# Kernel optimization log

Measured on AMD Instinct MI355X. Metric: run time of the kernel, lower is better.

## Reference

```python
import jax, jax.numpy as jnp
import numpy as np
import math

N_HEAD = 16
N_KV_HEAD = 4
WINDOW = 512
EPS = 1e-6


def _rotate_half(t):
    t1, t2 = jnp.split(t, 2, axis=-1)
    return jnp.concatenate([-t2, t1], axis=-1)


def _rope_tables(T, head_dim):
    theta = 1.0 / (10000.0 ** (jnp.arange(0, head_dim, 2, dtype=jnp.float32) / head_dim))
    pos = jnp.arange(T, dtype=jnp.float32)
    freqs = jnp.outer(pos, theta)                      # [T, d/2]
    cos = jnp.concatenate([jnp.cos(freqs), jnp.cos(freqs)], axis=-1)  # [T, d]
    sin = jnp.concatenate([jnp.sin(freqs), jnp.sin(freqs)], axis=-1)
    return cos, sin


def setup_inputs() -> dict:
    key = jax.random.key(0)
    k1, k2, k3, k4 = jax.random.split(key, 4)
    B, T, C = 1, 2048, 1024
    kv_out = 2 * N_KV_HEAD * (C // N_HEAD)  # 512
    x = jax.random.normal(k1, (B, T, C), dtype=jnp.float32)
    Wq = jax.random.normal(k2, (C, C), dtype=jnp.float32) * 0.02
    Wkv = jax.random.normal(k3, (kv_out, C), dtype=jnp.float32) * 0.02
    Wproj = jax.random.normal(k4, (C, C), dtype=jnp.float32) * 0.02
    return {"x": x, "Wq": Wq, "Wkv": Wkv, "Wproj": Wproj}


def reference(x, Wq, Wkv, Wproj):
    B, T, C = x.shape
    H, KV = N_HEAD, N_KV_HEAD
    d = C // H
    n_rep = H // KV

    q = (x @ Wq.T).reshape(B, T, H, d).transpose(0, 2, 1, 3)     # [B,H,T,d]
    kv = x @ Wkv.T                                               # [B,T,2*KV*d]
    k, v = jnp.split(kv, 2, axis=2)
    k = k.reshape(B, T, KV, d).transpose(0, 2, 1, 3)             # [B,KV,T,d]
    v = v.reshape(B, T, KV, d).transpose(0, 2, 1, 3)

    # QK L2 normalization
    q = q / (jnp.linalg.norm(q, axis=-1, keepdims=True) + EPS)
    k = k / (jnp.linalg.norm(k, axis=-1, keepdims=True) + EPS)

    # RoPE
    cos, sin = _rope_tables(T, d)
    cos = cos[None, None]  # [1,1,T,d]
    sin = sin[None, None]
    q = q * cos + _rotate_half(q) * sin
    k = k * cos + _rotate_half(k) * sin

    # GQA: repeat KV heads (repeat_interleave on head dim)
    k = jnp.repeat(k, n_rep, axis=1)   # [B,H,T,d]
    v = jnp.repeat(v, n_rep, axis=1)

    # sliding-window causal mask: cols <= rows and cols > rows - WINDOW
    rows = jnp.arange(T)[:, None]
    cols = jnp.arange(T)[None, :]
    mask = (cols <= rows) & (cols > rows - WINDOW)  # [T,T] bool

    scale = 1.0 / math.sqrt(d)
    scores = jnp.einsum("bhqd,bhkd->bhqk", q, k) * scale
    scores = jnp.where(mask[None, None], scores, -jnp.inf)
    attn = jax.nn.softmax(scores, axis=-1)
    y = jnp.einsum("bhqk,bhkd->bhqd", attn, v)      # [B,H,T,d]
    y = y.transpose(0, 2, 1, 3).reshape(B, T, C)
    return y @ Wproj.T
```

## Files before the change

kernel.cpp:

```cpp
#include <hip/hip_runtime.h>

#define T_SEQ 2048
#define C_DIM 1024
#define NH    16
#define NKV   4
#define HD    64
#define WIN   512

typedef __bf16 bf16x8 __attribute__((ext_vector_type(8)));
typedef __bf16 bf16x4 __attribute__((ext_vector_type(4)));
typedef float f32x4 __attribute__((ext_vector_type(4)));

#define MFMA16(a, b, c) __builtin_amdgcn_mfma_f32_16x16x32_bf16(a, b, c, 0, 0, 0)

#define GLD16(g, s)                                                          \
  __builtin_amdgcn_global_load_lds(                                          \
      (const __attribute__((address_space(1))) void*)(g),                    \
      (__attribute__((address_space(3))) void*)(s), 16, 0, 0)

__global__ __launch_bounds__(256) void prep_kernel(const float* __restrict__ x,
                                                   const float* __restrict__ Wq,
                                                   const float* __restrict__ Wkv,
                                                   const float* __restrict__ Wp,
                                                   __bf16* __restrict__ xb,
                                                   __bf16* __restrict__ Wqkvb,
                                                   __bf16* __restrict__ Wpb,
                                                   float2* __restrict__ ropeT) {
  int b = blockIdx.x;
  if (b >= 4608) {
    int idx = (b - 4608) * 256 + threadIdx.x;
    int t = idx >> 5, i = idx & 31;
    float theta = exp2f(-(float)i * (13.287712379549449f / 32.0f));
    float s, c;
    sincosf((float)t * theta, &s, &c);
    ropeT[idx] = make_float2(c, s);
    return;
  }
  const float* src;
  __bf16* dst;
  int off;
  if (b < 2048)      { src = x;   dst = xb;                off = b; }
  else if (b < 3072) { src = Wq;  dst = Wqkvb;             off = b - 2048; }
  else if (b < 3584) { src = Wkv; dst = Wqkvb + (1 << 20); off = b - 3072; }
  else               { src = Wp;  dst = Wpb;               off = b - 3584; }
  int i = off * 1024 + threadIdx.x * 4;
  float4 v = *(const float4*)(src + i);
  bf16x4 o;
  o[0] = (__bf16)v.x; o[1] = (__bf16)v.y; o[2] = (__bf16)v.z; o[3] = (__bf16)v.w;
  *(bf16x4*)(dst + i) = o;
}

__device__ __forceinline__ void gemm_core64(const __bf16* __restrict__ A,
                                            const __bf16* __restrict__ B,
                                            int K,
                                            __bf16* AsB, __bf16* BsB,
                                            f32x4 (&acc)[4]) {
  const int tid = threadIdx.x;
  const int w = tid >> 6, l = tid & 63;
  const int quad = l >> 4, r16 = l & 15;
  const int srow = w * 16 + (l >> 3);
  const size_t soff = (size_t)srow * K + (size_t)(((l & 7) ^ (l >> 3)) * 8);
  const __bf16* gA = A + soff;
  const __bf16* gB = B + soff;
  __bf16* const lA = AsB + w * 1024;
  __bf16* const lB = BsB + w * 1024;
  const size_t rstep = (size_t)8 * K;
  int rA[2], rB[4][2];
#pragma unroll
  for (int ks = 0; ks < 2; ++ks) {
    int row = w * 16 + r16;
    rA[ks] = row * 64 + (((ks * 4 + quad) ^ (row & 7)) * 8);
  }
#pragma unroll
  for (int nt = 0; nt < 4; ++nt)
#pragma unroll
    for (int ks = 0; ks < 2; ++ks) {
      int row = nt * 16 + r16;
      rB[nt][ks] = row * 64 + (((ks * 4 + quad) ^ (row & 7)) * 8);
    }
  const int nIter = K >> 6;
  GLD16(gA, lA);
  GLD16(gA + rstep, lA + 512);
  GLD16(gB, lB);
  GLD16(gB + rstep, lB + 512);
  __syncthreads();
  int cur = 0;
  for (int it = 0; it < nIter; ++it) {
    if (it + 1 < nIter) {
      const __bf16* ga = gA + ((it + 1) << 6);
      const __bf16* gb = gB + ((it + 1) << 6);
      __bf16* la = lA + ((cur ^ 1) << 12);
      __bf16* lb = lB + ((cur ^ 1) << 12);
      GLD16(ga, la);
      GLD16(ga + rstep, la + 512);
      GLD16(gb, lb);
      GLD16(gb + rstep, lb + 512);
    }
    const __bf16* Asc = AsB + (cur << 12);
    const __bf16* Bsc = BsB + (cur << 12);
#pragma unroll
    for (int ks = 0; ks < 2; ++ks) {
      bf16x8 fa  = *(const bf16x8*)(Asc + rA[ks]);
      bf16x8 fb0 = *(const bf16x8*)(Bsc + rB[0][ks]);
      bf16x8 fb1 = *(const bf16x8*)(Bsc + rB[1][ks]);
      bf16x8 fb2 = *(const bf16x8*)(Bsc + rB[2][ks]);
      bf16x8 fb3 = *(const bf16x8*)(Bsc + rB[3][ks]);
      acc[0] = MFMA16(fa, fb0, acc[0]);
      acc[1] = MFMA16(fa, fb1, acc[1]);
      acc[2] = MFMA16(fa, fb2, acc[2]);
      acc[3] = MFMA16(fa, fb3, acc[3]);
    }
    if (it + 1 < nIter) {
      __syncthreads();
      cur ^= 1;
    }
  }
}

__global__ __launch_bounds__(256) void gemm_qkv_kernel(const __bf16* __restrict__ xb,
                                                       const __bf16* __restrict__ Wqkvb,
                                                       const float2* __restrict__ ropeT,
                                                       __bf16* __restrict__ Qb,
                                                       __bf16* __restrict__ Kb,
                                                       __bf16* __restrict__ Vt) {
  __shared__ __align__(16) __bf16 smem[16384];
  __bf16* AsB = smem;
  __bf16* BsB = smem + 8192;
  f32x4 acc[4] = {};
  const int m0 = blockIdx.y * 64, n0 = blockIdx.x * 64;
  gemm_core64(xb + (size_t)m0 * C_DIM, Wqkvb + (size_t)n0 * C_DIM, C_DIM, AsB, BsB, acc);
  const int tid = threadIdx.x;
  const int w = tid >> 6, l = tid & 63, quad = l >> 4, r16 = l & 15;
  if (n0 < 1280) {
    const bool isQ = n0 < 1024;
    const int head = isQ ? (n0 >> 6) : ((n0 - 1024) >> 6);
    __bf16* dstBase = (isQ ? Qb : Kb) + (size_t)head * T_SEQ * HD;
    const float osc = isQ ? 0.125f : 1.0f;
#pragma unroll
    for (int r = 0; r < 4; ++r) {
      float ss = acc[0][r] * acc[0][r] + acc[1][r] * acc[1][r] +
                 acc[2][r] * acc[2][r] + acc[3][r] * acc[3][r];
#pragma unroll
      for (int m = 1; m < 16; m <<= 1) ss += __shfl_xor(ss, m, 64);
      const float inv = osc / (sqrtf(ss) + 1e-6f);
      const int t = m0 + w * 16 + quad * 4 + r;
      const float2 cs0 = ropeT[t * 32 + r16];
      const float2 cs1 = ropeT[t * 32 + 16 + r16];
      const float v0 = acc[0][r] * inv, v1 = acc[1][r] * inv;
      const float v2 = acc[2][r] * inv, v3 = acc[3][r] * inv;
      __bf16* dst = dstBase + (size_t)t * HD;
      dst[r16]      = (__bf16)(v0 * cs0.x - v2 * cs0.y);
      dst[16 + r16] = (__bf16)(v1 * cs1.x - v3 * cs1.y);
      dst[32 + r16] = (__bf16)(v2 * cs0.x + v0 * cs0.y);
      dst[48 + r16] = (__bf16)(v3 * cs1.x + v1 * cs1.y);
    }
  } else {
    const int kvh = (n0 - 1280) >> 6;
    __syncthreads();
    __bf16* Vs = smem;
#pragma unroll
    for (int nt = 0; nt < 4; ++nt)
#pragma unroll
      for (int r = 0; r < 4; ++r)
        Vs[(nt * 16 + r16) * 136 + w * 16 + quad * 4 + r] = (__bf16)acc[nt][r];
    __syncthreads();
    const int d = tid >> 2, tc = (tid & 3) * 16;
    __bf16* dst = Vt + ((size_t)kvh * HD + d) * T_SEQ + m0 + tc;
    bf16x8 v0 = *(const bf16x8*)(Vs + d * 136 + tc);
    bf16x8 v1 = *(const bf16x8*)(Vs + d * 136 + tc + 8);
    *(bf16x8*)dst = v0;
    *(bf16x8*)(dst + 8) = v1;
  }
}

__global__ __launch_bounds__(256) void gemm_proj_kernel(const __bf16* __restrict__ Yb,
                                                        const __bf16* __restrict__ Wpb,
                                                        float* __restrict__ C) {
  __shared__ __align__(16) __bf16 smem[16384];
  __bf16* AsB = smem;
  __bf16* BsB = smem + 8192;
  f32x4 acc[4] = {};
  const int m0 = blockIdx.y * 64, n0 = blockIdx.x * 64;
  gemm_core64(Yb + (size_t)m0 * C_DIM, Wpb + (size_t)n0 * C_DIM, C_DIM, AsB, BsB, acc);
  const int tid = threadIdx.x;
  const int w = tid >> 6, l = tid & 63, quad = l >> 4, r16 = l & 15;
  const int mrow = m0 + w * 16 + quad * 4;
  const int ncol = n0 + r16;
#pragma unroll
  for (int r = 0; r < 4; ++r) {
    size_t rowoff = (size_t)(mrow + r) * C_DIM;
    C[rowoff + ncol]      = acc[0][r];
    C[rowoff + ncol + 16] = acc[1][r];
    C[rowoff + ncol + 32] = acc[2][r];
    C[rowoff + ncol + 48] = acc[3][r];
  }
}

__global__ __launch_bounds__(256) void attn_mfma_kernel(const __bf16* __restrict__ Qb,
                                                        const __bf16* __restrict__ Kb,
                                                        const __bf16* __restrict__ Vt,
                                                        __bf16* __restrict__ Yb) {
  __shared__ __align__(16) __bf16 KVs[2][8192];
  __shared__ __align__(16) __bf16 Pl[4][16][72];
  const int h = blockIdx.y, kvh = h >> 2;
  const int t0 = blockIdx.x * 64;
  const int tid = threadIdx.x;
  const int w = tid >> 6, l = tid & 63;
  const int quad = l >> 4, r16 = l & 15;
  const int rr = l >> 3;
  const int cc = (l & 7) ^ rr;
  const __bf16* qptr = Qb + ((size_t)h * T_SEQ + t0 + w * 16 + r16) * HD + quad * 8;
  bf16x8 aq0 = *(const bf16x8*)(qptr);
  bf16x8 aq1 = *(const bf16x8*)(qptr + 32);
  const int keyStart = max(0, t0 - (WIN - 1)) & ~63;
  const int nch = ((t0 + 64) - keyStart) >> 6;
  const __bf16* kbase = Kb + (size_t)kvh * T_SEQ * HD;
  const __bf16* vbase = Vt + (size_t)kvh * HD * T_SEQ;
  const int tq = t0 + w * 16 + quad * 4;
  f32x4 oacc[4] = {};
  float lsum[4] = {0.f, 0.f, 0.f, 0.f};

  {
    __bf16* kd = &KVs[0][w * 1024];
    __bf16* vd = &KVs[0][4096 + w * 1024];
    const __bf16* kg = kbase + (size_t)(keyStart + w * 16 + rr) * HD + cc * 8;
    const __bf16* vg = vbase + (size_t)(w * 16 + rr) * T_SEQ + keyStart + cc * 8;
    GLD16(kg, kd); GLD16(kg + 8 * HD, kd + 512);
    GLD16(vg, vd); GLD16(vg + 8 * T_SEQ, vd + 512);
  }
  __syncthreads();
  int buf = 0;
  for (int it = 0; it < nch; ++it) {
    const int key0 = keyStart + (it << 6);
    if (it + 1 < nch) {
      const int kn = key0 + 64;
      __bf16* kd = &KVs[buf ^ 1][w * 1024];
      __bf16* vd = &KVs[buf ^ 1][4096 + w * 1024];
      const __bf16* kg = kbase + (size_t)(kn + w * 16 + rr) * HD + cc * 8;
      const __bf16* vg = vbase + (size_t)(w * 16 + rr) * T_SEQ + kn + cc * 8;
      GLD16(kg, kd); GLD16(kg + 8 * HD, kd + 512);
      GLD16(vg, vd); GLD16(vg + 8 * T_SEQ, vd + 512);
    }
    const __bf16* Ksc = &KVs[buf][0];
    const __bf16* Vsc = &KVs[buf][4096];
    f32x4 s[4] = {};
#pragma unroll
    for (int nt = 0; nt < 4; ++nt) {
      const int row = nt * 16 + r16;
      bf16x8 bk0 = *(const bf16x8*)(Ksc + row * 64 + ((quad ^ (row & 7)) * 8));
      bf16x8 bk1 = *(const bf16x8*)(Ksc + row * 64 + (((4 + quad) ^ (row & 7)) * 8));
      s[nt] = MFMA16(aq0, bk0, s[nt]);
      s[nt] = MFMA16(aq1, bk1, s[nt]);
    }
#pragma unroll
    for (int nt = 0; nt < 4; ++nt) {
      const int key = key0 + nt * 16 + r16;
#pragma unroll
      for (int r = 0; r < 4; ++r) {
        bool valid = (key <= tq + r) && (key > tq + r - WIN);
        float p = valid ? __expf(s[nt][r]) : 0.0f;
        lsum[r] += p;
        Pl[w][quad * 4 + r][nt * 16 + r16] = (__bf16)p;
      }
    }
    bf16x8 ap0 = *(const bf16x8*)(&Pl[w][r16][quad * 8]);
    bf16x8 ap1 = *(const bf16x8*)(&Pl[w][r16][32 + quad * 8]);
#pragma unroll
    for (int nt = 0; nt < 4; ++nt) {
      const int d = nt * 16 + r16;
      bf16x8 bv0 = *(const bf16x8*)(Vsc + d * 64 + ((quad ^ (d & 7)) * 8));
      bf16x8 bv1 = *(const bf16x8*)(Vsc + d * 64 + (((4 + quad) ^ (d & 7)) * 8));
      oacc[nt] = MFMA16(ap0, bv0, oacc[nt]);
      oacc[nt] = MFMA16(ap1, bv1, oacc[nt]);
    }
    __syncthreads();
    buf ^= 1;
  }
#pragma unroll
  for (int r = 0; r < 4; ++r) {
#pragma unroll
    for (int m = 1; m < 16; m <<= 1) lsum[r] += __shfl_xor(lsum[r], m, 64);
  }
#pragma unroll
  for (int r = 0; r < 4; ++r) {
    const float inv = 1.0f / lsum[r];
    const size_t row = (size_t)(tq + r);
#pragma unroll
    for (int nt = 0; nt < 4; ++nt)
      Yb[row * C_DIM + h * HD + nt * 16 + r16] = (__bf16)(oacc[nt][r] * inv);
  }
}

extern "C" void kernel_launch(void* const* d_in, const int* in_sizes, int n_in,
                              void* d_out, int out_size, void* d_ws, size_t ws_size,
                              hipStream_t stream) {
  const float* x     = (const float*)d_in[0];
  const float* Wq    = (const float*)d_in[1];
  const float* Wkv   = (const float*)d_in[2];
  const float* Wproj = (const float*)d_in[3];
  float* out = (float*)d_out;

  __bf16* xb    = (__bf16*)d_ws;
  __bf16* Wqkvb = xb + (size_t)T_SEQ * C_DIM;
  __bf16* Wpb   = Wqkvb + (size_t)1536 * C_DIM;
  __bf16* Qb    = Wpb + (size_t)C_DIM * C_DIM;
  __bf16* Kb    = Qb + (size_t)NH * T_SEQ * HD;
  __bf16* Vt    = Kb + (size_t)NKV * T_SEQ * HD;
  __bf16* Yb    = Vt + (size_t)NKV * HD * T_SEQ;
  float2* ropeT = (float2*)(Yb + (size_t)T_SEQ * C_DIM);

  prep_kernel<<<4864, 256, 0, stream>>>(x, Wq, Wkv, Wproj, xb, Wqkvb, Wpb, ropeT);
  gemm_qkv_kernel<<<dim3(24, 32), 256, 0, stream>>>(xb, Wqkvb, ropeT, Qb, Kb, Vt);
  attn_mfma_kernel<<<dim3(T_SEQ / 64, NH), 256, 0, stream>>>(Qb, Kb, Vt, Yb);
  gemm_proj_kernel<<<dim3(16, 32), 256, 0, stream>>>(Yb, Wpb, out);
}
```

Measured before the change: 107.3 us.

## Switch GEMM core to 32x32 MFMA with split-K across waves and LDS reduction

After: 424.9 us. 3.96x slower.

```diff
diff --git a/kernel.cpp b/kernel.cpp
--- a/kernel.cpp
+++ b/kernel.cpp
@@ -10,8 +10,10 @@
 typedef __bf16 bf16x8 __attribute__((ext_vector_type(8)));
 typedef __bf16 bf16x4 __attribute__((ext_vector_type(4)));
 typedef float f32x4 __attribute__((ext_vector_type(4)));
+typedef float f32x16 __attribute__((ext_vector_type(16)));
 
 #define MFMA16(a, b, c) __builtin_amdgcn_mfma_f32_16x16x32_bf16(a, b, c, 0, 0, 0)
+#define MFMA32(a, b, c) __builtin_amdgcn_mfma_f32_32x32x16_bf16(a, b, c, 0, 0, 0)
 
 #define GLD16(g, s)                                                          \
   __builtin_amdgcn_global_load_lds(                                          \
@@ -53,36 +55,30 @@
 __device__ __forceinline__ void gemm_core64(const __bf16* __restrict__ A,
                                             const __bf16* __restrict__ B,
                                             int K,
-                                            __bf16* AsB, __bf16* BsB,
-                                            f32x4 (&acc)[4]) {
+                                            __bf16* smem,
+                                            f32x16 (&acc)[2][2]) {
   const int tid = threadIdx.x;
   const int w = tid >> 6, l = tid & 63;
-  const int quad = l >> 4, r16 = l & 15;
+  const int hi = l >> 5, c = l & 31;
   const int srow = w * 16 + (l >> 3);
   const size_t soff = (size_t)srow * K + (size_t)(((l & 7) ^ (l >> 3)) * 8);
   const __bf16* gA = A + soff;
   const __bf16* gB = B + soff;
+  __bf16* AsB = smem;
+  __bf16* BsB = smem + 8192;
   __bf16* const lA = AsB + w * 1024;
   __bf16* const lB = BsB + w * 1024;
   const size_t rstep = (size_t)8 * K;
-  int rA[2], rB[4][2];
-#pragma unroll
-  for (int ks = 0; ks < 2; ++ks) {
-    int row = w * 16 + r16;
-    rA[ks] = row * 64 + (((ks * 4 + quad) ^ (row & 7)) * 8);
-  }
-#pragma unroll
-  for (int nt = 0; nt < 4; ++nt)
-#pragma unroll
-    for (int ks = 0; ks < 2; ++ks) {
-      int row = nt * 16 + r16;
-      rB[nt][ks] = row * 64 + (((ks * 4 + quad) ^ (row & 7)) * 8);
-    }
+  const int sc = w * 2 + hi;
+  int off[2];
+#pragma unroll
+  for (int mi = 0; mi < 2; ++mi) {
+    int row = c + mi * 32;
+    off[mi] = row * 64 + ((sc ^ (row & 7)) * 8);
+  }
   const int nIter = K >> 6;
-  GLD16(gA, lA);
-  GLD16(gA + rstep, lA + 512);
-  GLD16(gB, lB);
-  GLD16(gB + rstep, lB + 512);
+  GLD16(gA, lA); GLD16(gA + rstep, lA + 512);
+  GLD16(gB, lB); GLD16(gB + rstep, lB + 512);
   __syncthreads();
   int cur = 0;
   for (int it = 0; it < nIter; ++it) {
@@ -91,30 +87,77 @@
       const __bf16* gb = gB + ((it + 1) << 6);
       __bf16* la = lA + ((cur ^ 1) << 12);
       __bf16* lb = lB + ((cur ^ 1) << 12);
-      GLD16(ga, la);
-      GLD16(ga + rstep, la + 512);
-      GLD16(gb, lb);
-      GLD16(gb + rstep, lb + 512);
+      GLD16(ga, la); GLD16(ga + rstep, la + 512);
+      GLD16(gb, lb); GLD16(gb + rstep, lb + 512);
     }
     const __bf16* Asc = AsB + (cur << 12);
     const __bf16* Bsc = BsB + (cur << 12);
-#pragma unroll
-    for (int ks = 0; ks < 2; ++ks) {
-      bf16x8 fa  = *(const bf16x8*)(Asc + rA[ks]);
-      bf16x8 fb0 = *(const bf16x8*)(Bsc + rB[0][ks]);
-      bf16x8 fb1 = *(const bf16x8*)(Bsc + rB[1][ks]);
-      bf16x8 fb2 = *(const bf16x8*)(Bsc + rB[2][ks]);
-      bf16x8 fb3 = *(const bf16x8*)(Bsc + rB[3][ks]);
-      acc[0] = MFMA16(fa, fb0, acc[0]);
-      acc[1] = MFMA16(fa, fb1, acc[1]);
-      acc[2] = MFMA16(fa, fb2, acc[2]);
-      acc[3] = MFMA16(fa, fb3, acc[3]);
-    }
+    bf16x8 a0 = *(const bf16x8*)(Asc + off[0]);
+    bf16x8 a1 = *(const bf16x8*)(Asc + off[1]);
+    bf16x8 b0 = *(const bf16x8*)(Bsc + off[0]);
+    bf16x8 b1 = *(const bf16x8*)(Bsc + off[1]);
+    acc[0][0] = MFMA32(a0, b0, acc[0][0]);
+    acc[0][1] = MFMA32(a0, b1, acc[0][1]);
+    acc[1][0] = MFMA32(a1, b0, acc[1][0]);
+    acc[1][1] = MFMA32(a1, b1, acc[1][1]);
     if (it + 1 < nIter) {
       __syncthreads();
       cur ^= 1;
     }
   }
+  __syncthreads();
+  float* R0 = (float*)smem;
+  float* R1 = (float*)smem + 4096;
+  if (w >= 2) {
+    float* R = (w == 2) ? R0 : R1;
+#pragma unroll
+    for (int mi = 0; mi < 2; ++mi)
+#pragma unroll
+      for (int nj = 0; nj < 2; ++nj)
+#pragma unroll
+        for (int g = 0; g < 16; ++g) {
+          int row = (g & 3) + 8 * (g >> 2) + 4 * hi + mi * 32;
+          R[row * 64 + nj * 32 + c] = acc[mi][nj][g];
+        }
+  }
+  __syncthreads();
+  if (w < 2) {
+    const float* R = (w == 0) ? R0 : R1;
+#pragma unroll
+    for (int mi = 0; mi < 2; ++mi)
+#pragma unroll
+      for (int nj = 0; nj < 2; ++nj)
+#pragma unroll
+        for (int g = 0; g < 16; ++g) {
+          int row = (g & 3) + 8 * (g >> 2) + 4 * hi + mi * 32;
+          acc[mi][nj][g] += R[row * 64 + nj * 32 + c];
+        }
+  }
+  __syncthreads();
+  if (w < 2) {
+    float* Rw = (w == 0) ? R1 : R0;
+    const int mi = 1 - w;
+#pragma unroll
+    for (int nj = 0; nj < 2; ++nj)
+#pragma unroll
+      for (int g = 0; g < 16; ++g) {
+        int rl = (g & 3) + 8 * (g >> 2) + 4 * hi;
+        Rw[rl * 64 + nj * 32 + c] = acc[mi][nj][g];
+      }
+  }
+  __syncthreads();
+  if (w < 2) {
+    const float* Rr = (w == 0) ? R0 : R1;
+    const int mi = w;
+#pragma unroll
+    for (int nj = 0; nj < 2; ++nj)
+#pragma unroll
+      for (int g = 0; g < 16; ++g) {
+        int rl = (g & 3) + 8 * (g >> 2) + 4 * hi;
+        acc[mi][nj][g] += Rr[rl * 64 + nj * 32 + c];
+      }
+  }
+  __syncthreads();
 }
 
 __global__ __launch_bounds__(256) void gemm_qkv_kernel(const __bf16* __restrict__ xb,
@@ -124,50 +167,49 @@
                                                        __bf16* __restrict__ Kb,
                                                        __bf16* __restrict__ Vt) {
   __shared__ __align__(16) __bf16 smem[16384];
-  __bf16* AsB = smem;
-  __bf16* BsB = smem + 8192;
-  f32x4 acc[4] = {};
+  f32x16 acc[2][2] = {};
   const int m0 = blockIdx.y * 64, n0 = blockIdx.x * 64;
-  gemm_core64(xb + (size_t)m0 * C_DIM, Wqkvb + (size_t)n0 * C_DIM, C_DIM, AsB, BsB, acc);
+  gemm_core64(xb + (size_t)m0 * C_DIM, Wqkvb + (size_t)n0 * C_DIM, C_DIM, smem, acc);
   const int tid = threadIdx.x;
-  const int w = tid >> 6, l = tid & 63, quad = l >> 4, r16 = l & 15;
+  const int w = tid >> 6, l = tid & 63, hi = l >> 5, c = l & 31;
   if (n0 < 1280) {
     const bool isQ = n0 < 1024;
     const int head = isQ ? (n0 >> 6) : ((n0 - 1024) >> 6);
     __bf16* dstBase = (isQ ? Qb : Kb) + (size_t)head * T_SEQ * HD;
     const float osc = isQ ? 0.125f : 1.0f;
-#pragma unroll
-    for (int r = 0; r < 4; ++r) {
-      float ss = acc[0][r] * acc[0][r] + acc[1][r] * acc[1][r] +
-                 acc[2][r] * acc[2][r] + acc[3][r] * acc[3][r];
-#pragma unroll
-      for (int m = 1; m < 16; m <<= 1) ss += __shfl_xor(ss, m, 64);
-      const float inv = osc / (sqrtf(ss) + 1e-6f);
-      const int t = m0 + w * 16 + quad * 4 + r;
-      const float2 cs0 = ropeT[t * 32 + r16];
-      const float2 cs1 = ropeT[t * 32 + 16 + r16];
-      const float v0 = acc[0][r] * inv, v1 = acc[1][r] * inv;
-      const float v2 = acc[2][r] * inv, v3 = acc[3][r] * inv;
-      __bf16* dst = dstBase + (size_t)t * HD;
-      dst[r16]      = (__bf16)(v0 * cs0.x - v2 * cs0.y);
-      dst[16 + r16] = (__bf16)(v1 * cs1.x - v3 * cs1.y);
-      dst[32 + r16] = (__bf16)(v2 * cs0.x + v0 * cs0.y);
-      dst[48 + r16] = (__bf16)(v3 * cs1.x + v1 * cs1.y);
+    if (w < 2) {
+#pragma unroll
+      for (int g = 0; g < 16; ++g) {
+        float a0 = acc[w][0][g], a1 = acc[w][1][g];
+        float ss = a0 * a0 + a1 * a1;
+#pragma unroll
+        for (int m = 1; m < 32; m <<= 1) ss += __shfl_xor(ss, m, 64);
+        const float inv = osc / (sqrtf(ss) + 1e-6f);
+        const int t = m0 + (g & 3) + 8 * (g >> 2) + 4 * hi + w * 32;
+        const float2 cs = ropeT[t * 32 + c];
+        const float v0 = a0 * inv, v1 = a1 * inv;
+        __bf16* dst = dstBase + (size_t)t * HD;
+        dst[c]      = (__bf16)(v0 * cs.x - v1 * cs.y);
+        dst[c + 32] = (__bf16)(v1 * cs.x + v0 * cs.y);
+      }
     }
   } else {
     const int kvh = (n0 - 1280) >> 6;
-    __syncthreads();
     __bf16* Vs = smem;
-#pragma unroll
-    for (int nt = 0; nt < 4; ++nt)
-#pragma unroll
-      for (int r = 0; r < 4; ++r)
-        Vs[(nt * 16 + r16) * 136 + w * 16 + quad * 4 + r] = (__bf16)acc[nt][r];
+    if (w < 2) {
+#pragma unroll
+      for (int nj = 0; nj < 2; ++nj)
+#pragma unroll
+        for (int g = 0; g < 16; ++g) {
+          int row = (g & 3) + 8 * (g >> 2) + 4 * hi + w * 32;
+          Vs[(nj * 32 + c) * 72 + row] = (__bf16)acc[w][nj][g];
+        }
+    }
     __syncthreads();
     const int d = tid >> 2, tc = (tid & 3) * 16;
     __bf16* dst = Vt + ((size_t)kvh * HD + d) * T_SEQ + m0 + tc;
-    bf16x8 v0 = *(const bf16x8*)(Vs + d * 136 + tc);
-    bf16x8 v1 = *(const bf16x8*)(Vs + d * 136 + tc + 8);
+    bf16x8 v0 = *(const bf16x8*)(Vs + d * 72 + tc);
+    bf16x8 v1 = *(const bf16x8*)(Vs + d * 72 + tc + 8);
     *(bf16x8*)dst = v0;
     *(bf16x8*)(dst + 8) = v1;
   }
@@ -177,22 +219,19 @@
                                                         const __bf16* __restrict__ Wpb,
                                                         float* __restrict__ C) {
   __shared__ __align__(16) __bf16 smem[16384];
-  __bf16* AsB = smem;
-  __bf16* BsB = smem + 8192;
-  f32x4 acc[4] = {};
+  f32x16 acc[2][2] = {};
   const int m0 = blockIdx.y * 64, n0 = blockIdx.x * 64;
-  gemm_core64(Yb + (size_t)m0 * C_DIM, Wpb + (size_t)n0 * C_DIM, C_DIM, AsB, BsB, acc);
+  gemm_core64(Yb + (size_t)m0 * C_DIM, Wpb + (size_t)n0 * C_DIM, C_DIM, smem, acc);
   const int tid = threadIdx.x;
-  const int w = tid >> 6, l = tid & 63, quad = l >> 4, r16 = l & 15;
-  const int mrow = m0 + w * 16 + quad * 4;
-  const int ncol = n0 + r16;
-#pragma unroll
-  for (int r = 0; r < 4; ++r) {
-    size_t rowoff = (size_t)(mrow + r) * C_DIM;
-    C[rowoff + ncol]      = acc[0][r];
-    C[rowoff + ncol + 16] = acc[1][r];
-    C[rowoff + ncol + 32] = acc[2][r];
-    C[rowoff + ncol + 48] = acc[3][r];
+  const int w = tid >> 6, l = tid & 63, hi = l >> 5, c = l & 31;
+  if (w < 2) {
+#pragma unroll
+    for (int nj = 0; nj < 2; ++nj)
+#pragma unroll
+      for (int g = 0; g < 16; ++g) {
+        const int row = (g & 3) + 8 * (g >> 2) + 4 * hi + w * 32;
+        C[(size_t)(m0 + row) * C_DIM + n0 + nj * 32 + c] = acc[w][nj][g];
+      }
   }
 }
 
```
